# Kernel tuning notes

Measured on AMD Instinct MI355X. Metric: run time of the kernel, lower is better.

## Reference

```python
import jax, jax.numpy as jnp
import numpy as np

B, S, E, H = 2, 2048, 1024, 16
HD = E // H


def setup_inputs() -> dict:
    key = jax.random.key(0)
    ks = jax.random.split(key, 5)
    scale = 1.0 / np.sqrt(E)
    return {
        "x": jax.random.normal(ks[0], (B, S, E), dtype=jnp.float32),
        "Wq": jax.random.normal(ks[1], (H, HD, E), dtype=jnp.float32) * scale,
        "Wk": jax.random.normal(ks[2], (H, HD, E), dtype=jnp.float32) * scale,
        "Wv": jax.random.normal(ks[3], (H, HD, E), dtype=jnp.float32) * scale,
        "Wo": jax.random.normal(ks[4], (E, E), dtype=jnp.float32) * scale,
    }


def reference(x, Wq, Wk, Wv, Wo):
    # Batched per-head projections: torch Linear y = x @ W.T, W: [head_dim, E]
    q = jnp.einsum("bse,hde->bshd", x, Wq)  # [B,S,H,HD]
    k = jnp.einsum("bse,hde->bshd", x, Wk)
    v = jnp.einsum("bse,hde->bshd", x, Wv)
    # Scaled dot-product attention; original scales by sqrt(head_dim)
    scores = jnp.einsum("bqhd,bkhd->bhqk", q, k) / jnp.sqrt(jnp.float32(HD))
    attn = jax.nn.softmax(scores, axis=-1)  # [B,H,S,S]
    out_h = jnp.einsum("bhqk,bkhd->bqhd", attn, v)  # [B,S,H,HD]
    out_cat = out_h.reshape(x.shape[0], x.shape[1], -1)  # concat heads -> [B,S,E]
    return out_cat @ Wo.T
```

## Files before the change

### kernel.cpp

```cpp
#include <hip/hip_runtime.h>
#include <hip/hip_bf16.h>

typedef unsigned short u16;
typedef unsigned int u32;
typedef __attribute__((ext_vector_type(4))) float f32x4;
typedef __attribute__((ext_vector_type(16))) float f32x16;
typedef __attribute__((ext_vector_type(8))) short short8;
typedef __attribute__((ext_vector_type(8))) unsigned short u16x8;
typedef __attribute__((ext_vector_type(4))) unsigned short u16x4;
typedef __attribute__((ext_vector_type(4))) unsigned int u32x4;

#define BATCH 2
#define SEQ   2048
#define EMB   1024
#define NH    16
#define HD    64

__device__ inline u16 f2bf(float f) {
    unsigned u = __builtin_bit_cast(unsigned, f);
    unsigned r = u + 0x7FFFu + ((u >> 16) & 1u);
    return (u16)(r >> 16);
}

__device__ inline float fexp2(float x) {
    float r;
    asm("v_exp_f32 %0, %1" : "=v"(r) : "v"(x));
    return r;
}

__device__ inline void gload16(const void* g, void* l) {
    __builtin_amdgcn_global_load_lds(
        (const __attribute__((address_space(1))) unsigned int*)g,
        (__attribute__((address_space(3))) unsigned int*)l, 16, 0, 0);
}

__device__ inline short8 mk8(u32 a, u32 b, u32 c, u32 d) {
    u32x4 t; t[0] = a; t[1] = b; t[2] = c; t[3] = d;
    return __builtin_bit_cast(short8, t);
}

#define PACK_ST(st, w0,w1,w2,w3,w4,w5,w6,w7)                                   \
  {                                                                            \
    asm("v_cvt_pk_bf16_f32 %0, %1, %2" : "=v"(w0) : "v"(st[0]),  "v"(st[1]));  \
    asm("v_cvt_pk_bf16_f32 %0, %1, %2" : "=v"(w1) : "v"(st[2]),  "v"(st[3]));  \
    asm("v_cvt_pk_bf16_f32 %0, %1, %2" : "=v"(w2) : "v"(st[4]),  "v"(st[5]));  \
    asm("v_cvt_pk_bf16_f32 %0, %1, %2" : "=v"(w3) : "v"(st[6]),  "v"(st[7]));  \
    asm("v_permlane32_swap_b32 %0, %1" : "+v"(w0), "+v"(w2));                  \
    asm("v_permlane32_swap_b32 %0, %1" : "+v"(w1), "+v"(w3));                  \
    asm("v_cvt_pk_bf16_f32 %0, %1, %2" : "=v"(w4) : "v"(st[8]),  "v"(st[9]));  \
    asm("v_cvt_pk_bf16_f32 %0, %1, %2" : "=v"(w5) : "v"(st[10]), "v"(st[11])); \
    asm("v_cvt_pk_bf16_f32 %0, %1, %2" : "=v"(w6) : "v"(st[12]), "v"(st[13])); \
    asm("v_cvt_pk_bf16_f32 %0, %1, %2" : "=v"(w7) : "v"(st[14]), "v"(st[15])); \
    asm("v_permlane32_swap_b32 %0, %1" : "+v"(w4), "+v"(w6));                  \
    asm("v_permlane32_swap_b32 %0, %1" : "+v"(w5), "+v"(w7));                  \
  }

__global__ __launch_bounds__(256) void convert_all(
    const float* __restrict__ x,
    const float* __restrict__ Wq, const float* __restrict__ Wk, const float* __restrict__ Wv,
    u16* __restrict__ Xb, u16* __restrict__ Wqkv)
{
    const long gidx = (long)blockIdx.x * 2048 + (long)threadIdx.x * 8;
    const float* src;
    u16* dst;
    if (gidx < 4194304L) {
        src = x + gidx; dst = Xb + gidx;
    } else {
        const long r = gidx - 4194304L;
        const int w = (int)(r >> 20);
        const long off = r & 1048575L;
        src = (w == 0 ? Wq : w == 1 ? Wk : Wv) + off;
        dst = Wqkv + r;
    }
    f32x4 a = *(const f32x4*)src;
    f32x4 b = *(const f32x4*)(src + 4);
    u16x8 o;
    #pragma unroll
    for (int j = 0; j < 4; ++j) { o[j] = f2bf(a[j]); o[4 + j] = f2bf(b[j]); }
    *(u16x8*)dst = o;
}

__global__ __launch_bounds__(256) void convert_wo(
    const float* __restrict__ Wo, u16* __restrict__ Wob)
{
    const long gidx = (long)blockIdx.x * 2048 + (long)threadIdx.x * 8;
    f32x4 a = *(const f32x4*)(Wo + gidx);
    f32x4 b = *(const f32x4*)(Wo + gidx + 4);
    u16x8 o;
    #pragma unroll
    for (int j = 0; j < 4; ++j) { o[j] = f2bf(a[j]); o[4 + j] = f2bf(b[j]); }
    *(u16x8*)(Wob + gidx) = o;
}

__global__ __launch_bounds__(512, 2) void gemm256(
    const u16* __restrict__ A, const u16* __restrict__ Bb,
    u16* __restrict__ Qo, u16* __restrict__ Ko, u16* __restrict__ VTo)
{
    __shared__ u16 As[2][256 * 64];
    __shared__ u16 Bs[2][256 * 64];

    const int tid = threadIdx.x;
    const int lane = tid & 63;
    const int wid = tid >> 6;
    const int lr = lane & 15;
    const int lg = lane >> 4;
    const int wr = wid >> 2;
    const int wc = wid & 3;

    const int lin = blockIdx.y * 16 + blockIdx.x;
    const int swz = (lin & 7) * 24 + (lin >> 3);
    const int m0 = (swz & 15) * 256;
    const int n0 = (swz >> 4) * 256;

    const int grow = lane >> 3;
    const int schunk = ((lane & 7) ^ grow) << 4;

    auto issueTile = [&](int kt, int buf) {
        const int k0b = kt * 128;
        #pragma unroll
        for (int i = 0; i < 4; ++i) {
            const int row = i * 64 + wid * 8 + grow;
            gload16((const char*)A + (size_t)(m0 + row) * 2048 + k0b + schunk,
                    (char*)As[buf] + i * 8192 + wid * 1024);
            gload16((const char*)Bb + (size_t)(n0 + row) * 2048 + k0b + schunk,
                    (char*)Bs[buf] + i * 8192 + wid * 1024);
        }
    };

    issueTile(0, 0);
    issueTile(1, 1);

    f32x4 acc[8][4] = {};
    const int rsw = (lr & 7);

    for (int t = 0; t < 16; ++t) {
        if (t < 15) { asm volatile("s_waitcnt vmcnt(8)" ::: "memory"); }
        else        { asm volatile("s_waitcnt vmcnt(0)" ::: "memory"); }
        __builtin_amdgcn_sched_barrier(0);
        __builtin_amdgcn_s_barrier();
        __builtin_amdgcn_sched_barrier(0);

        const u16* Ac = As[t & 1];
        const u16* Bc = Bs[t & 1];

        short8 a[4][2], b0[2][2], b1[2][2];

        #pragma unroll
        for (int fi = 0; fi < 4; ++fi)
            #pragma unroll
            for (int ks = 0; ks < 2; ++ks)
                a[fi][ks] = *(const short8*)((const char*)Ac + (wr * 128 + fi * 16 + lr) * 128
                                             + (((ks * 4 + lg) ^ rsw) << 4));
        #pragma unroll
        for (int fj = 0; fj < 2; ++fj)
            #pragma unroll
            for (int ks = 0; ks < 2; ++ks)
                b0[fj][ks] = *(const short8*)((const char*)Bc + (wc * 64 + fj * 16 + lr) * 128
                                              + (((ks * 4 + lg) ^ rsw) << 4));
        __builtin_amdgcn_s_setprio(1);
        #pragma unroll
        for (int fi = 0; fi < 4; ++fi)
            #pragma unroll
            for (int fj = 0; fj < 2; ++fj)
                #pragma unroll
                for (int ks = 0; ks < 2; ++ks)
                    acc[fi][fj] = __builtin_amdgcn_mfma_f32_16x16x32_bf16(a[fi][ks], b0[fj][ks], acc[fi][fj], 0, 0, 0);
        __builtin_amdgcn_s_setprio(0);

        #pragma unroll
        for (int fj = 0; fj < 2; ++fj)
            #pragma unroll
            for (int ks = 0; ks < 2; ++ks)
                b1[fj][ks] = *(const short8*)((const char*)Bc + (wc * 64 + (fj + 2) * 16 + lr) * 128
                                              + (((ks * 4 + lg) ^ rsw) << 4));
        __builtin_amdgcn_s_setprio(1);
        #pragma unroll
        for (int fi = 0; fi < 4; ++fi)
            #pragma unroll
            for (int fj = 0; fj < 2; ++fj)
                #pragma unroll
                for (int ks = 0; ks < 2; ++ks)
                    acc[fi][fj + 2] = __builtin_amdgcn_mfma_f32_16x16x32_bf16(a[fi][ks], b1[fj][ks], acc[fi][fj + 2], 0, 0, 0);
        __builtin_amdgcn_s_setprio(0);

        #pragma unroll
        for (int fi = 0; fi < 4; ++fi)
            #pragma unroll
            for (int ks = 0; ks < 2; ++ks)
                a[fi][ks] = *(const short8*)((const char*)Ac + (wr * 128 + (fi + 4) * 16 + lr) * 128
                                             + (((ks * 4 + lg) ^ rsw) << 4));
        __builtin_amdgcn_s_setprio(1);
        #pragma unroll
        for (int fi = 0; fi < 4; ++fi)
            #pragma unroll
            for (int fj = 0; fj < 2; ++fj)
                #pragma unroll
                for (int ks = 0; ks < 2; ++ks)
                    acc[fi + 4][fj + 2] = __builtin_amdgcn_mfma_f32_16x16x32_bf16(a[fi][ks], b1[fj][ks], acc[fi + 4][fj + 2], 0, 0, 0);
        __builtin_amdgcn_s_setprio(0);

        __builtin_amdgcn_s_setprio(1);
        #pragma unroll
        for (int fi = 0; fi < 4; ++fi)
            #pragma unroll
            for (int fj = 0; fj < 2; ++fj)
                #pragma unroll
                for (int ks = 0; ks < 2; ++ks)
                    acc[fi + 4][fj] = __builtin_amdgcn_mfma_f32_16x16x32_bf16(a[fi][ks], b0[fj][ks], acc[fi + 4][fj], 0, 0, 0);
        __builtin_amdgcn_s_setprio(0);

        __builtin_amdgcn_sched_barrier(0);
        __builtin_amdgcn_s_barrier();
        __builtin_amdgcn_sched_barrier(0);
        if (t + 2 < 16) issueTile(t + 2, t & 1);
    }

    const int w = n0 >> 10;
    const float qs = (w == 0) ? 0.125f * 1.44269504f : 1.0f;
    const int mb = m0 + wr * 128;
    const int nb = n0 + wc * 64;
    #pragma unroll
    for (int fi = 0; fi < 8; ++fi) {
        #pragma unroll
        for (int fj = 0; fj < 4; ++fj) {
            const int m = mb + fi * 16 + lg * 4;
            const int nn = (nb + fj * 16 + lr) & 1023;
            const int h = nn >> 6, d = nn & 63;
            const int bb = m >> 11, s = m & 2047;
            const size_t bh = (size_t)(bb * NH + h);
            if (w == 2) {
                u16x4 v;
                #pragma unroll
                for (int i = 0; i < 4; ++i) v[i] = f2bf(acc[fi][fj][i]);
                *(u16x4*)&VTo[(bh * HD + d) * SEQ + s] = v;
            } else {
                u16* P = (w == 0) ? Qo : Ko;
                #pragma unroll
                for (int i = 0; i < 4; ++i)
                    P[(bh * SEQ + s + i) * HD + d] = f2bf(acc[fi][fj][i] * qs);
            }
        }
    }
}

__global__ __launch_bounds__(256) void gemm_out(
    const u16* __restrict__ A, const u16* __restrict__ Bb, float* __restrict__ Fo)
{
    __shared__ u16 As[2][128 * 64];
    __shared__ u16 Bs[2][128 * 64];

    const int tid = threadIdx.x;

    const int lin = blockIdx.y * 32 + blockIdx.x;
    const int swz = (lin & 7) * 32 + (lin >> 3);
    const int m0 = (swz & 31) * 128;
    const int n0 = (swz >> 5) * 128;

    const int lane = tid & 63;
    const int lr = lane & 15;
    const int lg = lane >> 4;
    const int wid = tid >> 6;
    const int wm = wid >> 1, wn = wid & 1;

    const int grow = lane >> 3;
    const int gcolb = ((lane & 7) ^ grow) << 4;
    const int rswz = (lr & 7);

    f32x4 acc[4][4] = {};

    auto issue = [&](int kt, int buf) {
        const int k0b = kt * 128;
        #pragma unroll
        for (int t = 0; t < 4; ++t) {
            const int row = (wid * 4 + t) * 8 + grow;
            gload16((const char*)A + (size_t)(m0 + row) * 2048 + k0b + gcolb,
                    (char*)As[buf] + (wid * 4 + t) * 1024);
            gload16((const char*)Bb + (size_t)(n0 + row) * 2048 + k0b + gcolb,
                    (char*)Bs[buf] + (wid * 4 + t) * 1024);
        }
    };

    issue(0, 0);
    issue(1, 1);

    for (int kt = 0; kt < 16; ++kt) {
        if (kt < 15) { asm volatile("s_waitcnt vmcnt(8)" ::: "memory"); }
        else         { asm volatile("s_waitcnt vmcnt(0)" ::: "memory"); }
        __builtin_amdgcn_sched_barrier(0);
        __builtin_amdgcn_s_barrier();
        __builtin_amdgcn_sched_barrier(0);

        const u16* Ac = As[kt & 1];
        const u16* Bc = Bs[kt & 1];
        #pragma unroll
        for (int kk = 0; kk < 2; ++kk) {
            short8 a[4], b[4];
            #pragma unroll
            for (int i = 0; i < 4; ++i)
                a[i] = *(const short8*)((const char*)Ac + (wm * 64 + i * 16 + lr) * 128
                                        + (((kk * 4 + lg) ^ rswz) << 4));
            #pragma unroll
            for (int i = 0; i < 4; ++i)
                b[i] = *(const short8*)((const char*)Bc + (wn * 64 + i * 16 + lr) * 128
                                        + (((kk * 4 + lg) ^ rswz) << 4));
            #pragma unroll
            for (int mi = 0; mi < 4; ++mi)
                #pragma unroll
                for (int ni = 0; ni < 4; ++ni)
                    acc[mi][ni] = __builtin_amdgcn_mfma_f32_16x16x32_bf16(a[mi], b[ni], acc[mi][ni], 0, 0, 0);
        }

        __builtin_amdgcn_sched_barrier(0);
        __builtin_amdgcn_s_barrier();
        __builtin_amdgcn_sched_barrier(0);
        if (kt + 2 < 16) issue(kt + 2, kt & 1);
    }

    const int mb = m0 + wm * 64;
    const int nb = n0 + wn * 64;
    #pragma unroll
    for (int mi = 0; mi < 4; ++mi)
        #pragma unroll
        for (int ni = 0; ni < 4; ++ni) {
            const int m = mb + mi * 16 + lg * 4;
            const int n = nb + ni * 16 + lr;
            #pragma unroll
            for (int i = 0; i < 4; ++i)
                Fo[(size_t)(m + i) * EMB + n] = acc[mi][ni][i];
        }
}

__global__ __launch_bounds__(512) void attn_fwd(
    const u16* __restrict__ Q, const u16* __restrict__ K,
    const u16* __restrict__ VT, u16* __restrict__ Cat)
{
    __shared__ u16 Ks[2][64 * 64];
    __shared__ u16 Vs[2][64 * 64];

    const int tid = threadIdx.x;
    const int lane = tid & 63;
    const int wid = tid >> 6;
    const int lq = lane & 31;
    const int hi = lane >> 5;

    const int lin = blockIdx.y * 8 + blockIdx.x;
    const int swz = (lin & 7) * 32 + (lin >> 3);
    const int qt = swz & 7;
    const int bh = swz >> 3;
    const int b = bh >> 4, h = bh & 15;

    const u16* Qg = Q + ((size_t)bh * SEQ + qt * 256 + wid * 32 + lq) * HD;
    short8 qf[4];
    #pragma unroll
    for (int ks = 0; ks < 4; ++ks)
        qf[ks] = *(const short8*)((const char*)Qg + ks * 32 + hi * 16);

    float m = -1e30f, l = 0.f;
    f32x16 ot0 = {}, ot1 = {};

    const u16* Kg = K + (size_t)bh * SEQ * HD;
    const u16* Vg = VT + (size_t)bh * HD * SEQ;

    const int srow = lane >> 3;
    const int schunk = ((lane & 7) ^ srow) << 4;

    auto issueKV = [&](int nt) {
        const int kv0 = nt * 64;
        const int krow = wid * 8 + srow;
        gload16((const char*)Kg + (size_t)(kv0 + krow) * 128 + schunk,
                (char*)Ks[nt & 1] + wid * 1024);
        gload16((const char*)Vg + (size_t)krow * (SEQ * 2) + kv0 * 2 + schunk,
                (char*)Vs[nt & 1] + wid * 1024);
    };

    issueKV(0);
    issueKV(1);

    const int rsw = (lq & 7);
    const int NT = SEQ / 64;
    for (int nt = 0; nt < NT; ++nt) {
        const int cur = nt & 1;
        if (nt < NT - 1) { asm volatile("s_waitcnt vmcnt(2)" ::: "memory"); }
        else             { asm volatile("s_waitcnt vmcnt(0)" ::: "memory"); }
        __builtin_amdgcn_sched_barrier(0);
        __builtin_amdgcn_s_barrier();
        __builtin_amdgcn_sched_barrier(0);

        f32x16 st0 = {}, st1 = {};
        #pragma unroll
        for (int ks = 0; ks < 4; ++ks) {
            const int co = ((ks * 2 + hi) ^ rsw) << 4;
            const short8 kf0 = *(const short8*)((const char*)Ks[cur] + lq * 128 + co);
            const short8 kf1 = *(const short8*)((const char*)Ks[cur] + (32 + lq) * 128 + co);
            st0 = __builtin_amdgcn_mfma_f32_32x32x16_bf16(kf0, qf[ks], st0, 0, 0, 0);
            st1 = __builtin_amdgcn_mfma_f32_32x32x16_bf16(kf1, qf[ks], st1, 0, 0, 0);
        }

        float mx = st0[0];
        #pragma unroll
        for (int i = 1; i < 16; ++i) mx = fmaxf(mx, st0[i]);
        #pragma unroll
        for (int i = 0; i < 16; ++i) mx = fmaxf(mx, st1[i]);
        mx = fmaxf(mx, __shfl_xor(mx, 32));
        if (!__all(mx - m <= 11.5f)) {
            const float nm = fmaxf(m, mx);
            const float corr = fexp2(m - nm);
            m = nm;
            l *= corr;
            #pragma unroll
            for (int i = 0; i < 16; ++i) { ot0[i] *= corr; ot1[i] *= corr; }
        }
        float rs = 0.f;
        #pragma unroll
        for (int i = 0; i < 16; ++i) {
            st0[i] = fexp2(st0[i] - m); rs += st0[i];
            st1[i] = fexp2(st1[i] - m); rs += st1[i];
        }
        rs += __shfl_xor(rs, 32);
        l += rs;

        u32 a0, a1, a2, a3, a4, a5, a6, a7;
        u32 c0, c1, c2, c3, c4, c5, c6, c7;
        PACK_ST(st0, a0, a1, a2, a3, a4, a5, a6, a7);
        PACK_ST(st1, c0, c1, c2, c3, c4, c5, c6, c7);
        const short8 pf0 = mk8(a0, a1, a2, a3);
        const short8 pf1 = mk8(a4, a5, a6, a7);
        const short8 pf2 = mk8(c0, c1, c2, c3);
        const short8 pf3 = mk8(c4, c5, c6, c7);

        #pragma unroll
        for (int ks = 0; ks < 4; ++ks) {
            const short8 pf = (ks == 0) ? pf0 : (ks == 1) ? pf1 : (ks == 2) ? pf2 : pf3;
            const int co = ((ks * 2 + hi) ^ rsw) << 4;
            const short8 vf0 = *(const short8*)((const char*)Vs[cur] + lq * 128 + co);
            const short8 vf1 = *(const short8*)((const char*)Vs[cur] + (32 + lq) * 128 + co);
            ot0 = __builtin_amdgcn_mfma_f32_32x32x16_bf16(vf0, pf, ot0, 0, 0, 0);
            ot1 = __builtin_amdgcn_mfma_f32_32x32x16_bf16(vf1, pf, ot1, 0, 0, 0);
        }

        __builtin_amdgcn_sched_barrier(0);
        __builtin_amdgcn_s_barrier();
        __builtin_amdgcn_sched_barrier(0);
        if (nt + 2 < NT) issueKV(nt + 2);
    }

    const float invl = 1.f / l;
    const int qrow = qt * 256 + wid * 32 + lq;
    u16* ob = Cat + ((size_t)b * SEQ + qrow) * EMB + h * HD;
    #pragma unroll
    for (int g = 0; g < 4; ++g) {
        u16x4 o0, o1;
        #pragma unroll
        for (int i = 0; i < 4; ++i) {
            o0[i] = f2bf(ot0[g * 4 + i] * invl);
            o1[i] = f2bf(ot1[g * 4 + i] * invl);
        }
        *(u16x4*)&ob[g * 8 + hi * 4] = o0;
        *(u16x4*)&ob[32 + g * 8 + hi * 4] = o1;
    }
}

extern "C" void kernel_launch(void* const* d_in, const int* in_sizes, int n_in,
                              void* d_out, int out_size, void* d_ws, size_t ws_size,
                              hipStream_t stream) {
    const float* x  = (const float*)d_in[0];
    const float* Wq = (const float*)d_in[1];
    const float* Wk = (const float*)d_in[2];
    const float* Wv = (const float*)d_in[3];
    const float* Wo = (const float*)d_in[4];
    float* out = (float*)d_out;

    u16* Xb   = (u16*)d_out;
    u16* Wqkv = (u16*)d_out + (size_t)4 * 1048576;

    char* ws = (char*)d_ws;
    u16* Qb  = (u16*)(ws);
    u16* Kb  = (u16*)(ws + (size_t)8  * 1048576);
    u16* VTb = (u16*)(ws + (size_t)16 * 1048576);
    u16* Cat = (u16*)(ws + (size_t)24 * 1048576);
    u16* Wob = Qb;

    convert_all<<<3584, 256, 0, stream>>>(x, Wq, Wk, Wv, Xb, Wqkv);

    dim3 g1(4096 / 256, 3072 / 256);
    gemm256<<<g1, 512, 0, stream>>>(Xb, Wqkv, Qb, Kb, VTb);

    dim3 g2(SEQ / 256, BATCH * NH);
    attn_fwd<<<g2, 512, 0, stream>>>(Qb, Kb, VTb, Cat);

    convert_wo<<<512, 256, 0, stream>>>(Wo, Wob);
    dim3 g3(4096 / 128, 1024 / 128);
    gemm_out<<<g3, 256, 0, stream>>>(Cat, Wob, out);
}
```

Before: 129.0 us.

## Halve attention block size to 128 queries and tree-reduce softmax max/sum

```diff
diff --git a/kernel.cpp b/kernel.cpp
--- a/kernel.cpp
+++ b/kernel.cpp
@@ -330,7 +330,7 @@
         }
 }
 
-__global__ __launch_bounds__(512) void attn_fwd(
+__global__ __launch_bounds__(256) void attn_fwd(
     const u16* __restrict__ Q, const u16* __restrict__ K,
     const u16* __restrict__ VT, u16* __restrict__ Cat)
 {
@@ -343,13 +343,13 @@
     const int lq = lane & 31;
     const int hi = lane >> 5;
 
-    const int lin = blockIdx.y * 8 + blockIdx.x;
-    const int swz = (lin & 7) * 32 + (lin >> 3);
-    const int qt = swz & 7;
-    const int bh = swz >> 3;
+    const int lin = blockIdx.y * 16 + blockIdx.x;
+    const int swz = (lin & 7) * 64 + (lin >> 3);
+    const int qt = swz & 15;
+    const int bh = swz >> 4;
     const int b = bh >> 4, h = bh & 15;
 
-    const u16* Qg = Q + ((size_t)bh * SEQ + qt * 256 + wid * 32 + lq) * HD;
+    const u16* Qg = Q + ((size_t)bh * SEQ + qt * 128 + wid * 32 + lq) * HD;
     short8 qf[4];
     #pragma unroll
     for (int ks = 0; ks < 4; ++ks)
@@ -366,11 +366,14 @@
 
     auto issueKV = [&](int nt) {
         const int kv0 = nt * 64;
-        const int krow = wid * 8 + srow;
-        gload16((const char*)Kg + (size_t)(kv0 + krow) * 128 + schunk,
-                (char*)Ks[nt & 1] + wid * 1024);
-        gload16((const char*)Vg + (size_t)krow * (SEQ * 2) + kv0 * 2 + schunk,
-                (char*)Vs[nt & 1] + wid * 1024);
+        #pragma unroll
+        for (int i = 0; i < 2; ++i) {
+            const int krow = i * 32 + wid * 8 + srow;
+            gload16((const char*)Kg + (size_t)(kv0 + krow) * 128 + schunk,
+                    (char*)Ks[nt & 1] + i * 4096 + wid * 1024);
+            gload16((const char*)Vg + (size_t)krow * (SEQ * 2) + kv0 * 2 + schunk,
+                    (char*)Vs[nt & 1] + i * 4096 + wid * 1024);
+        }
     };
 
     issueKV(0);
@@ -380,7 +383,7 @@
     const int NT = SEQ / 64;
     for (int nt = 0; nt < NT; ++nt) {
         const int cur = nt & 1;
-        if (nt < NT - 1) { asm volatile("s_waitcnt vmcnt(2)" ::: "memory"); }
+        if (nt < NT - 1) { asm volatile("s_waitcnt vmcnt(4)" ::: "memory"); }
         else             { asm volatile("s_waitcnt vmcnt(0)" ::: "memory"); }
         __builtin_amdgcn_sched_barrier(0);
         __builtin_amdgcn_s_barrier();
@@ -396,12 +399,16 @@
             st1 = __builtin_amdgcn_mfma_f32_32x32x16_bf16(kf1, qf[ks], st1, 0, 0, 0);
         }
 
-        float mx = st0[0];
-        #pragma unroll
-        for (int i = 1; i < 16; ++i) mx = fmaxf(mx, st0[i]);
-        #pragma unroll
-        for (int i = 0; i < 16; ++i) mx = fmaxf(mx, st1[i]);
-        mx = fmaxf(mx, __shfl_xor(mx, 32));
+        float tr[16];
+        #pragma unroll
+        for (int i = 0; i < 8; ++i) tr[i] = fmaxf(st0[2 * i], st0[2 * i + 1]);
+        #pragma unroll
+        for (int i = 0; i < 8; ++i) tr[8 + i] = fmaxf(st1[2 * i], st1[2 * i + 1]);
+        #pragma unroll
+        for (int s = 8; s > 0; s >>= 1)
+            #pragma unroll
+            for (int i = 0; i < s; ++i) tr[i] = fmaxf(tr[i], tr[i + s]);
+        float mx = fmaxf(tr[0], __shfl_xor(tr[0], 32));
         if (!__all(mx - m <= 11.5f)) {
             const float nm = fmaxf(m, mx);
             const float corr = fexp2(m - nm);
@@ -410,14 +417,20 @@
             #pragma unroll
             for (int i = 0; i < 16; ++i) { ot0[i] *= corr; ot1[i] *= corr; }
         }
-        float rs = 0.f;
         #pragma unroll
         for (int i = 0; i < 16; ++i) {
-            st0[i] = fexp2(st0[i] - m); rs += st0[i];
-            st1[i] = fexp2(st1[i] - m); rs += st1[i];
-        }
-        rs += __shfl_xor(rs, 32);
-        l += rs;
+            st0[i] = fexp2(st0[i] - m);
+            st1[i] = fexp2(st1[i] - m);
+        }
+        #pragma unroll
+        for (int i = 0; i < 8; ++i) tr[i] = st0[2 * i] + st0[2 * i + 1];
+        #pragma unroll
+        for (int i = 0; i < 8; ++i) tr[8 + i] = st1[2 * i] + st1[2 * i + 1];
+        #pragma unroll
+        for (int s = 8; s > 0; s >>= 1)
+            #pragma unroll
+            for (int i = 0; i < s; ++i) tr[i] += tr[i + s];
+        l += tr[0] + __shfl_xor(tr[0], 32);
 
         u32 a0, a1, a2, a3, a4, a5, a6, a7;
         u32 c0, c1, c2, c3, c4, c5, c6, c7;
@@ -445,7 +458,7 @@
     }
 
     const float invl = 1.f / l;
-    const int qrow = qt * 256 + wid * 32 + lq;
+    const int qrow = qt * 128 + wid * 32 + lq;
     u16* ob = Cat + ((size_t)b * SEQ + qrow) * EMB + h * HD;
     #pragma unroll
     for (int g = 0; g < 4; ++g) {
@@ -485,8 +498,8 @@
     dim3 g1(4096 / 256, 3072 / 256);
     gemm256<<<g1, 512, 0, stream>>>(Xb, Wqkv, Qb, Kb, VTb);
 
-    dim3 g2(SEQ / 256, BATCH * NH);
-    attn_fwd<<<g2, 512, 0, stream>>>(Qb, Kb, VTb, Cat);
+    dim3 g2(SEQ / 128, BATCH * NH);
+    attn_fwd<<<g2, 256, 0, stream>>>(Qb, Kb, VTb, Cat);
 
     convert_wo<<<512, 256, 0, stream>>>(Wo, Wob);
     dim3 g3(4096 / 128, 1024 / 128);
```

Result: no change. 128.5 us (-0.5%).
